# Kernel optimization log

Measured on AMD Instinct MI355X. Metric: run time of the kernel, lower is better.

The kernel has to match this reference:

```python
import jax, jax.numpy as jnp
import numpy as np

N_HEADS, N_KV, HEAD_DIM, D_MODEL, T_MAX = 16, 4, 64, 1024, 2048
GROUPS = N_HEADS // N_KV
EPS = 1e-6


def _rms_norm(x, w):
    # RMSNorm over last dim (head_dim), computed in fp32 like the torch module
    xf = x.astype(jnp.float32)
    r = jax.lax.rsqrt(jnp.mean(xf * xf, axis=-1, keepdims=True) + EPS)
    return (xf * r).astype(x.dtype) * w


def _apply_rope(x, cos, sin):
    # x: (B, H, T, D); cos/sin: (T_max, D/2)
    T = x.shape[2]
    c = cos[:T][None, None]  # (1,1,T,D/2)
    s = sin[:T][None, None]
    x1, x2 = jnp.split(x, 2, axis=-1)
    return jnp.concatenate([x1 * c - x2 * s, x2 * c + x1 * s], axis=-1)


def setup_inputs() -> dict:
    key = jax.random.key(0)
    ks = jax.random.split(key, 8)
    B, T = 2, 2048
    x = jax.random.normal(ks[0], (B, T, D_MODEL), dtype=jnp.float32)
    # realistic RoPE tables
    theta = 10000.0
    inv_freq = 1.0 / (theta ** (np.arange(0, HEAD_DIM, 2, dtype=np.float32) / HEAD_DIM))
    t = np.arange(T_MAX, dtype=np.float32)
    freqs = np.outer(t, inv_freq)  # (T_max, D/2)
    cos = jnp.asarray(np.cos(freqs))
    sin = jnp.asarray(np.sin(freqs))
    sd = 0.02
    wq = jax.random.normal(ks[1], (N_HEADS * HEAD_DIM, D_MODEL), dtype=jnp.float32) * sd
    wk = jax.random.normal(ks[2], (N_KV * HEAD_DIM, D_MODEL), dtype=jnp.float32) * sd
    wv = jax.random.normal(ks[3], (N_KV * HEAD_DIM, D_MODEL), dtype=jnp.float32) * sd
    wo = jax.random.normal(ks[4], (D_MODEL, N_HEADS * HEAD_DIM), dtype=jnp.float32) * sd
    qn_w = jnp.ones((HEAD_DIM,), dtype=jnp.float32)
    kn_w = jnp.ones((HEAD_DIM,), dtype=jnp.float32)
    return {"x": x, "cos": cos, "sin": sin, "wq": wq, "wk": wk, "wv": wv,
            "wo": wo, "qn_w": qn_w, "kn_w": kn_w}


def reference(x, cos, sin, wq, wk, wv, wo, qn_w, kn_w):
    B, T, _ = x.shape
    scale = HEAD_DIM ** -0.5
    # projections (torch Linear: y = x @ W.T)
    q = (x @ wq.T).reshape(B, T, N_HEADS, HEAD_DIM).transpose(0, 2, 1, 3)
    k = (x @ wk.T).reshape(B, T, N_KV, HEAD_DIM).transpose(0, 2, 1, 3)
    v = (x @ wv.T).reshape(B, T, N_KV, HEAD_DIM).transpose(0, 2, 1, 3)
    # qk RMSNorm
    q = _rms_norm(q, qn_w)
    k = _rms_norm(k, kn_w)
    # RoPE
    q = _apply_rope(q, cos, sin)
    k = _apply_rope(k, cos, sin)
    # GQA expansion: query head h uses kv head h // GROUPS
    k = jnp.repeat(k, GROUPS, axis=1)  # (B, H, T, D)
    v = jnp.repeat(v, GROUPS, axis=1)
    # causal SDPA
    scores = jnp.einsum('bhqd,bhkd->bhqk', q, k) * scale
    causal = jnp.tril(jnp.ones((T, T), dtype=bool))
    scores = jnp.where(causal, scores, jnp.finfo(scores.dtype).min)
    p = jax.nn.softmax(scores, axis=-1)
    out = jnp.einsum('bhqk,bhkd->bhqd', p, v)
    out = out.transpose(0, 2, 1, 3).reshape(B, T, N_HEADS * HEAD_DIM)
    return out @ wo.T
```

## Files before the change

kernel.cpp:

```cpp
#include <hip/hip_runtime.h>


typedef __bf16 bf16;
typedef __attribute__((ext_vector_type(8))) __bf16 bf16x8;
typedef __attribute__((ext_vector_type(4))) float f32x4;

#define MFMA(a, b, c) __builtin_amdgcn_mfma_f32_16x16x32_bf16((a), (b), (c), 0, 0, 0)
#define GLOAD_LDS16(g, l)                                        \
  __builtin_amdgcn_global_load_lds(                              \
      (const __attribute__((address_space(1))) void*)(g),        \
      (__attribute__((address_space(3))) void*)(l), 16, 0, 0)

__device__ __forceinline__ bool is_bf16_input(const void* cosRaw) {
  return ((const unsigned short*)cosRaw)[0] == 0x3F80;
}
__device__ __forceinline__ float rdval(const void* p, int idx, bool isbf) {
  return isbf ? (float)((const bf16*)p)[idx] : ((const float*)p)[idx];
}

__device__ __forceinline__ void stage_rows(const void* src, size_t rowbase,
                                           int ko, int srow, int csrc,
                                           int lane, bf16* ls, bool isbf) {
  if (isbf) {
    GLOAD_LDS16(&((const bf16*)src)[(rowbase + srow) * 1024 + ko + csrc * 8], ls);
  } else {
    const float* fp = &((const float*)src)[(rowbase + srow) * 1024 + ko + csrc * 8];
    float4 f0 = *(const float4*)fp;
    float4 f1 = *(const float4*)(fp + 4);
    bf16x8 o;
    o[0] = (bf16)f0.x; o[1] = (bf16)f0.y; o[2] = (bf16)f0.z; o[3] = (bf16)f0.w;
    o[4] = (bf16)f1.x; o[5] = (bf16)f1.y; o[6] = (bf16)f1.z; o[7] = (bf16)f1.w;
    *(bf16x8*)&ls[lane * 8] = o;
  }
}

__global__ __launch_bounds__(256, 6) void proj_kernel(
    const void* __restrict__ xraw, const void* __restrict__ wqraw,
    const void* __restrict__ wkraw, const void* __restrict__ wvraw,
    bf16* __restrict__ qp, bf16* __restrict__ kp, bf16* __restrict__ vt,
    const void* __restrict__ cosraw, const void* __restrict__ sinraw,
    const void* __restrict__ qnraw, const void* __restrict__ knraw) {
  __shared__ bf16 As[64 * 64];
  __shared__ bf16 Bs[64 * 64];

  const int idx = (int)blockIdx.x;
  const int xcd = idx & 7;
  const int jj = idx >> 3;
  const int mb = (jj & 7) * 8 + xcd;
  const int nb = jj >> 3;
  const int n0 = nb * 64;
  const int m0 = mb * 64;

  const int tid = threadIdx.x;
  const int wave = tid >> 6;
  const int lane = tid & 63;
  const int q16 = lane & 15;
  const int quad = lane >> 4;
  const int srow = lane >> 3;
  const int csrc = (lane & 7) ^ srow;
  const int wm = wave * 16;
  const int x7 = q16 & 7;
  const bool isbf = is_bf16_input(cosraw);

  const void* wsrc;
  int nr0;
  if (nb < 16)      { wsrc = wqraw; nr0 = n0; }
  else if (nb < 20) { wsrc = wkraw; nr0 = n0 - 1024; }
  else              { wsrc = wvraw; nr0 = n0 - 1280; }

  f32x4 acc[4];
#pragma unroll
  for (int nt = 0; nt < 4; ++nt) acc[nt] = (f32x4){0.f, 0.f, 0.f, 0.f};

  for (int kt = 0; kt < 16; ++kt) {
    const int ko = kt * 64;
#pragma unroll
    for (int i = 0; i < 2; ++i) {
      int rb = wave * 16 + i * 8;
      stage_rows(xraw, (size_t)(m0 + rb), ko, srow, csrc, lane, &As[rb * 64], isbf);
      stage_rows(wsrc, (size_t)(nr0 + rb), ko, srow, csrc, lane, &Bs[rb * 64], isbf);
    }
    __syncthreads();

    bf16x8 a0, a1, bfr[4][2];
    {
      const bf16* rp = &As[(wm + q16) * 64];
      a0 = *(const bf16x8*)&rp[(quad ^ x7) * 8];
      a1 = *(const bf16x8*)&rp[((quad + 4) ^ x7) * 8];
    }
#pragma unroll
    for (int nt = 0; nt < 4; ++nt) {
      const bf16* rp = &Bs[(nt * 16 + q16) * 64];
      bfr[nt][0] = *(const bf16x8*)&rp[(quad ^ x7) * 8];
      bfr[nt][1] = *(const bf16x8*)&rp[((quad + 4) ^ x7) * 8];
    }
#pragma unroll
    for (int nt = 0; nt < 4; ++nt) {
      acc[nt] = MFMA(a0, bfr[nt][0], acc[nt]);
      acc[nt] = MFMA(a1, bfr[nt][1], acc[nt]);
    }
    __syncthreads();
  }

  if (nb < 20) {
    const void* nwp = (nb < 16) ? qnraw : knraw;
    const float osc = (nb < 16) ? 0.125f : 1.0f;
    float wd[4];
#pragma unroll
    for (int nt = 0; nt < 4; ++nt) wd[nt] = rdval(nwp, nt * 16 + q16, isbf);

#pragma unroll
    for (int r = 0; r < 4; ++r) {
      float p = acc[0][r] * acc[0][r] + acc[1][r] * acc[1][r] +
                acc[2][r] * acc[2][r] + acc[3][r] * acc[3][r];
#pragma unroll
      for (int off = 8; off >= 1; off >>= 1) p += __shfl_xor(p, off);
      float rms = rsqrtf(p * (1.0f / 64.0f) + 1e-6f);

      int row = m0 + wm + quad * 4 + r;
      int t = row & 2047;
      float c0 = rdval(cosraw, t * 32 + q16, isbf);
      float c1 = rdval(cosraw, t * 32 + 16 + q16, isbf);
      float s0 = rdval(sinraw, t * 32 + q16, isbf);
      float s1 = rdval(sinraw, t * 32 + 16 + q16, isbf);

      float v0 = acc[0][r] * rms * wd[0];
      float v1 = acc[1][r] * rms * wd[1];
      float v2 = acc[2][r] * rms * wd[2];
      float v3 = acc[3][r] * rms * wd[3];

      bf16* op = (nb < 16) ? &qp[(size_t)row * 1024 + nb * 64]
                           : &kp[(size_t)row * 256 + (nb - 16) * 64];
      op[0 * 16 + q16] = (bf16)((v0 * c0 - v2 * s0) * osc);
      op[1 * 16 + q16] = (bf16)((v1 * c1 - v3 * s1) * osc);
      op[2 * 16 + q16] = (bf16)((v2 * c0 + v0 * s0) * osc);
      op[3 * 16 + q16] = (bf16)((v3 * c1 + v1 * s1) * osc);
    }
  } else {
    const int vh = nb - 20;
    const int b = m0 >> 11;
    const int tbase = m0 & 2047;
#pragma unroll
    for (int nt = 0; nt < 4; ++nt)
#pragma unroll
      for (int r = 0; r < 4; ++r)
        As[(wm + quad * 4 + r) * 64 + nt * 16 + q16] = (bf16)acc[nt][r];
    __syncthreads();
#pragma unroll
    for (int rep = 0; rep < 2; ++rep) {
      int c = tid + 256 * rep;
      int d = c >> 3;
      int t8 = (c & 7) * 8;
      bf16x8 pk;
#pragma unroll
      for (int j = 0; j < 8; ++j) pk[j] = As[(t8 + j) * 64 + d];
      *(bf16x8*)&vt[(((size_t)(b * 4 + vh)) * 64 + d) * 2048 + tbase + t8] = pk;
    }
  }
}

__global__ __launch_bounds__(256, 2) void flash_kernel(
    const bf16* __restrict__ qp, const bf16* __restrict__ kp,
    const bf16* __restrict__ vt, bf16* __restrict__ attn) {
  const int qblk = blockIdx.z ? 31 - (int)blockIdx.x : (int)blockIdx.x;
  const int hp = blockIdx.y;
  const int b = blockIdx.z;
  const int h0 = hp * 2;
  const int kvh = hp >> 1;
  const int tid = threadIdx.x;
  const int wave = tid >> 6;
  const int lane = tid & 63;
  const int q16 = lane & 15;
  const int quad = lane >> 4;
  const int r7 = q16 & 7;
  const int t0 = qblk * 64 + wave * 16;

  __shared__ bf16 Ks[2][64 * 64];
  __shared__ bf16 Vs[2][64 * 64];
  __shared__ bf16 Pl[4][2][16 * 64];

  bf16x8 qa[2][2];
#pragma unroll
  for (int hd = 0; hd < 2; ++hd) {
    const bf16* qrow =
        qp + (((size_t)(b * 2048 + t0 + q16)) * 16 + h0 + hd) * 64;
    qa[hd][0] = *(const bf16x8*)(qrow + quad * 8);
    qa[hd][1] = *(const bf16x8*)(qrow + 32 + quad * 8);
  }

  bf16x8 ones;
#pragma unroll
  for (int j = 0; j < 8; ++j) ones[j] = (bf16)1.0f;

  f32x4 O[2][4], l4[2];
#pragma unroll
  for (int hd = 0; hd < 2; ++hd) {
#pragma unroll
    for (int nt = 0; nt < 4; ++nt) O[hd][nt] = (f32x4){0.f, 0.f, 0.f, 0.f};
    l4[hd] = (f32x4){0.f, 0.f, 0.f, 0.f};
  }

  const int ntile = qblk + 1;

  bf16x8 kr[2], vr[2];
  const int cr = tid * 2;
  const int krow = cr >> 3;
  const size_t kgbase = (((size_t)(b * 2048) + krow) * 4 + kvh) * 64;
  const size_t vgbase = ((size_t)(b * 4 + kvh) * 64 + krow) * 2048;

  auto gload = [&](int tk) {
#pragma unroll
    for (int rep = 0; rep < 2; ++rep) {
      int ch = (cr + rep) & 7;
      kr[rep] = *(const bf16x8*)&kp[kgbase + (size_t)(tk * 64) * 256 + ch * 8];
      vr[rep] = *(const bf16x8*)&vt[vgbase + tk * 64 + ch * 8];
    }
  };
  auto swrite = [&](int bb) {
#pragma unroll
    for (int rep = 0; rep < 2; ++rep) {
      int ch = (cr + rep) & 7;
      int pos = (ch ^ (krow & 7)) * 8;
      *(bf16x8*)&Ks[bb][krow * 64 + pos] = kr[rep];
      *(bf16x8*)&Vs[bb][krow * 64 + pos] = vr[rep];
    }
  };

  gload(0);

  for (int t = 0; t < ntile; ++t) {
    const int bb = t & 1;
    const int kbase = t * 64;
    swrite(bb);
    __syncthreads();
    if (t + 1 < ntile) gload(t + 1);

    bf16x8 vbr[2][4];
#pragma unroll
    for (int kh = 0; kh < 2; ++kh)
#pragma unroll
      for (int nt = 0; nt < 4; ++nt) {
        const bf16* vr0 = &Vs[bb][(nt * 16 + q16) * 64];
        vbr[kh][nt] = *(const bf16x8*)&vr0[((kh * 4 + quad) ^ r7) * 8];
      }

    bf16x8 kb[4][2];
#pragma unroll
    for (int kt = 0; kt < 4; ++kt) {
      const bf16* kr0 = &Ks[bb][(kt * 16 + q16) * 64];
      kb[kt][0] = *(const bf16x8*)&kr0[(quad ^ r7) * 8];
      kb[kt][1] = *(const bf16x8*)&kr0[((quad + 4) ^ r7) * 8];
    }

    const bool edge = (kbase + 63 > t0);
#pragma unroll
    for (int hd = 0; hd < 2; ++hd) {
      f32x4 s[4];
#pragma unroll
      for (int kt = 0; kt < 4; ++kt) {
        f32x4 z = (f32x4){0.f, 0.f, 0.f, 0.f};
        z = MFMA(qa[hd][0], kb[kt][0], z);
        z = MFMA(qa[hd][1], kb[kt][1], z);
        s[kt] = z;
      }
      if (edge) {
#pragma unroll
        for (int kt = 0; kt < 4; ++kt) {
          int jt = kbase + kt * 16 + q16;
#pragma unroll
          for (int r = 0; r < 4; ++r)
            if (jt > t0 + quad * 4 + r) s[kt][r] = -1e30f;
        }
      }
#pragma unroll
      for (int kt = 0; kt < 4; ++kt)
#pragma unroll
        for (int r = 0; r < 4; ++r) s[kt][r] = __expf(s[kt][r] - 9.0f);

#pragma unroll
      for (int kt = 0; kt < 4; ++kt)
#pragma unroll
        for (int r = 0; r < 4; ++r) {
          int row = quad * 4 + r;
          int col = kt * 16 + q16;
          Pl[wave][hd][row * 64 + ((col >> 3) ^ (row & 7)) * 8 + (col & 7)] =
              (bf16)s[kt][r];
        }
    }

#pragma unroll
    for (int hd = 0; hd < 2; ++hd)
#pragma unroll
      for (int kh = 0; kh < 2; ++kh) {
        bf16x8 pa = *(const bf16x8*)&Pl[wave][hd][q16 * 64 +
                                                  (((kh * 4 + quad) ^ r7) * 8)];
#pragma unroll
        for (int nt = 0; nt < 4; ++nt)
          O[hd][nt] = MFMA(pa, vbr[kh][nt], O[hd][nt]);
        l4[hd] = MFMA(pa, ones, l4[hd]);
      }
  }

#pragma unroll
  for (int hd = 0; hd < 2; ++hd) {
    float inv[4];
#pragma unroll
    for (int r = 0; r < 4; ++r) inv[r] = 1.0f / l4[hd][r];
#pragma unroll
    for (int nt = 0; nt < 4; ++nt)
#pragma unroll
      for (int r = 0; r < 4; ++r) {
        size_t o = (((size_t)(b * 2048 + t0 + quad * 4 + r)) * 16 + h0 + hd) * 64 +
                   nt * 16 + q16;
        attn[o] = (bf16)(O[hd][nt][r] * inv[r]);
      }
  }
}

__global__ __launch_bounds__(256, 6) void gemm_o_kernel(
    const bf16* __restrict__ A, const void* __restrict__ Wraw,
    void* __restrict__ C, const void* __restrict__ cosraw) {
  __shared__ bf16 As[64 * 64];
  __shared__ bf16 Bs[64 * 64];

  const int idx = (int)blockIdx.x;
  const int xcd = idx & 7;
  const int jj = idx >> 3;
  const int mb = (jj & 7) * 8 + xcd;
  const int nb = jj >> 3;
  const int n0 = nb * 64;
  const int m0 = mb * 64;

  const int tid = threadIdx.x;
  const int wave = tid >> 6;
  const int lane = tid & 63;
  const int q16 = lane & 15;
  const int quad = lane >> 4;
  const int srow = lane >> 3;
  const int csrc = (lane & 7) ^ srow;
  const int wm = wave * 16;
  const int x7 = q16 & 7;
  const bool isbf = is_bf16_input(cosraw);

  f32x4 acc[4];
#pragma unroll
  for (int nt = 0; nt < 4; ++nt) acc[nt] = (f32x4){0.f, 0.f, 0.f, 0.f};

  for (int kt = 0; kt < 16; ++kt) {
    const int ko = kt * 64;
#pragma unroll
    for (int i = 0; i < 2; ++i) {
      int rb = wave * 16 + i * 8;
      GLOAD_LDS16(&A[(size_t)(m0 + rb + srow) * 1024 + ko + csrc * 8],
                  &As[rb * 64]);
      stage_rows(Wraw, (size_t)(n0 + rb), ko, srow, csrc, lane, &Bs[rb * 64], isbf);
    }
    __syncthreads();

    bf16x8 a0, a1, bfr[4][2];
    {
      const bf16* rp = &As[(wm + q16) * 64];
      a0 = *(const bf16x8*)&rp[(quad ^ x7) * 8];
      a1 = *(const bf16x8*)&rp[((quad + 4) ^ x7) * 8];
    }
#pragma unroll
    for (int nt = 0; nt < 4; ++nt) {
      const bf16* rp = &Bs[(nt * 16 + q16) * 64];
      bfr[nt][0] = *(const bf16x8*)&rp[(quad ^ x7) * 8];
      bfr[nt][1] = *(const bf16x8*)&rp[((quad + 4) ^ x7) * 8];
    }
#pragma unroll
    for (int nt = 0; nt < 4; ++nt) {
      acc[nt] = MFMA(a0, bfr[nt][0], acc[nt]);
      acc[nt] = MFMA(a1, bfr[nt][1], acc[nt]);
    }
    __syncthreads();
  }

#pragma unroll
  for (int nt = 0; nt < 4; ++nt)
#pragma unroll
    for (int r = 0; r < 4; ++r) {
      size_t idx2 = (size_t)(m0 + wm + quad * 4 + r) * 1024 + n0 + nt * 16 + q16;
      if (isbf) ((bf16*)C)[idx2] = (bf16)acc[nt][r];
      else      ((float*)C)[idx2] = acc[nt][r];
    }
}

extern "C" void kernel_launch(void* const* d_in, const int* in_sizes, int n_in,
                              void* d_out, int out_size, void* d_ws, size_t ws_size,
                              hipStream_t stream) {
  bf16* qp = (bf16*)d_ws;
  bf16* kp = qp + (size_t)4096 * 1024;
  bf16* vt = kp + (size_t)4096 * 256;
  bf16* at = vt + (size_t)4096 * 256;

  proj_kernel<<<1536, 256, 0, stream>>>(
      d_in[0], d_in[3], d_in[4], d_in[5], qp, kp, vt,
      d_in[1], d_in[2], d_in[7], d_in[8]);

  flash_kernel<<<dim3(32, 8, 2), 256, 0, stream>>>(qp, kp, vt, at);

  gemm_o_kernel<<<1024, 256, 0, stream>>>(at, d_in[6], d_out, d_in[1]);
}
```

Before: 176.8 us.

## Process one head per flash block to double grid and occupancy

The flash attention kernel now handles a single query head per block instead of two heads sharing a KV tile. The grid doubles along the head dimension and launch bounds rise to 4 blocks per CU. The P tile is written and consumed in 32-column halves interleaved with the PV MFMAs, which shrinks the LDS and register footprint. The trade-off is that each K/V tile is loaded from global memory twice as often, since two heads no longer share one staged tile.

```diff
diff --git a/kernel.cpp b/kernel.cpp
--- a/kernel.cpp
+++ b/kernel.cpp
@@ -159,14 +159,13 @@
   }
 }
 
-__global__ __launch_bounds__(256, 2) void flash_kernel(
+__global__ __launch_bounds__(256, 4) void flash_kernel(
     const bf16* __restrict__ qp, const bf16* __restrict__ kp,
     const bf16* __restrict__ vt, bf16* __restrict__ attn) {
   const int qblk = blockIdx.z ? 31 - (int)blockIdx.x : (int)blockIdx.x;
-  const int hp = blockIdx.y;
+  const int h = blockIdx.y;
   const int b = blockIdx.z;
-  const int h0 = hp * 2;
-  const int kvh = hp >> 1;
+  const int kvh = h >> 2;
   const int tid = threadIdx.x;
   const int wave = tid >> 6;
   const int lane = tid & 63;
@@ -177,28 +176,20 @@
 
   __shared__ bf16 Ks[2][64 * 64];
   __shared__ bf16 Vs[2][64 * 64];
-  __shared__ bf16 Pl[4][2][16 * 64];
-
-  bf16x8 qa[2][2];
-#pragma unroll
-  for (int hd = 0; hd < 2; ++hd) {
-    const bf16* qrow =
-        qp + (((size_t)(b * 2048 + t0 + q16)) * 16 + h0 + hd) * 64;
-    qa[hd][0] = *(const bf16x8*)(qrow + quad * 8);
-    qa[hd][1] = *(const bf16x8*)(qrow + 32 + quad * 8);
-  }
+  __shared__ bf16 Pl[4][16 * 32];
+
+  const bf16* qrow = qp + (((size_t)(b * 2048 + t0 + q16)) * 16 + h) * 64;
+  bf16x8 qa0 = *(const bf16x8*)(qrow + quad * 8);
+  bf16x8 qa1 = *(const bf16x8*)(qrow + 32 + quad * 8);
 
   bf16x8 ones;
 #pragma unroll
   for (int j = 0; j < 8; ++j) ones[j] = (bf16)1.0f;
 
-  f32x4 O[2][4], l4[2];
-#pragma unroll
-  for (int hd = 0; hd < 2; ++hd) {
-#pragma unroll
-    for (int nt = 0; nt < 4; ++nt) O[hd][nt] = (f32x4){0.f, 0.f, 0.f, 0.f};
-    l4[hd] = (f32x4){0.f, 0.f, 0.f, 0.f};
-  }
+  f32x4 O[4], l4;
+#pragma unroll
+  for (int nt = 0; nt < 4; ++nt) O[nt] = (f32x4){0.f, 0.f, 0.f, 0.f};
+  l4 = (f32x4){0.f, 0.f, 0.f, 0.f};
 
   const int ntile = qblk + 1;
 
@@ -235,86 +226,68 @@
     __syncthreads();
     if (t + 1 < ntile) gload(t + 1);
 
-    bf16x8 vbr[2][4];
-#pragma unroll
-    for (int kh = 0; kh < 2; ++kh)
+    f32x4 s[4];
+#pragma unroll
+    for (int kt = 0; kt < 4; ++kt) {
+      const bf16* kr0 = &Ks[bb][(kt * 16 + q16) * 64];
+      bf16x8 kb0 = *(const bf16x8*)&kr0[(quad ^ r7) * 8];
+      bf16x8 kb1 = *(const bf16x8*)&kr0[((quad + 4) ^ r7) * 8];
+      f32x4 z = (f32x4){0.f, 0.f, 0.f, 0.f};
+      z = MFMA(qa0, kb0, z);
+      z = MFMA(qa1, kb1, z);
+      s[kt] = z;
+    }
+
+    if (kbase + 63 > t0) {
+#pragma unroll
+      for (int kt = 0; kt < 4; ++kt) {
+        int jt = kbase + kt * 16 + q16;
+#pragma unroll
+        for (int r = 0; r < 4; ++r)
+          if (jt > t0 + quad * 4 + r) s[kt][r] = -1e30f;
+      }
+    }
+
+#pragma unroll
+    for (int kt = 0; kt < 4; ++kt)
+#pragma unroll
+      for (int r = 0; r < 4; ++r) s[kt][r] = __expf(s[kt][r] - 9.0f);
+
+#pragma unroll
+    for (int kh = 0; kh < 2; ++kh) {
+#pragma unroll
+      for (int ct = 0; ct < 2; ++ct) {
+        const int kt = kh * 2 + ct;
+#pragma unroll
+        for (int r = 0; r < 4; ++r) {
+          int row = quad * 4 + r;
+          int col = ct * 16 + q16;
+          Pl[wave][row * 32 + (((col >> 3) ^ (row & 3)) * 8) + (col & 7)] =
+              (bf16)s[kt][r];
+        }
+      }
+      bf16x8 pa = *(const bf16x8*)&Pl[wave][q16 * 32 + ((quad ^ (q16 & 3)) * 8)];
 #pragma unroll
       for (int nt = 0; nt < 4; ++nt) {
         const bf16* vr0 = &Vs[bb][(nt * 16 + q16) * 64];
-        vbr[kh][nt] = *(const bf16x8*)&vr0[((kh * 4 + quad) ^ r7) * 8];
+        bf16x8 vb = *(const bf16x8*)&vr0[((kh * 4 + quad) ^ r7) * 8];
+        O[nt] = MFMA(pa, vb, O[nt]);
       }
-
-    bf16x8 kb[4][2];
-#pragma unroll
-    for (int kt = 0; kt < 4; ++kt) {
-      const bf16* kr0 = &Ks[bb][(kt * 16 + q16) * 64];
-      kb[kt][0] = *(const bf16x8*)&kr0[(quad ^ r7) * 8];
-      kb[kt][1] = *(const bf16x8*)&kr0[((quad + 4) ^ r7) * 8];
-    }
-
-    const bool edge = (kbase + 63 > t0);
-#pragma unroll
-    for (int hd = 0; hd < 2; ++hd) {
-      f32x4 s[4];
-#pragma unroll
-      for (int kt = 0; kt < 4; ++kt) {
-        f32x4 z = (f32x4){0.f, 0.f, 0.f, 0.f};
-        z = MFMA(qa[hd][0], kb[kt][0], z);
-        z = MFMA(qa[hd][1], kb[kt][1], z);
-        s[kt] = z;
-      }
-      if (edge) {
-#pragma unroll
-        for (int kt = 0; kt < 4; ++kt) {
-          int jt = kbase + kt * 16 + q16;
-#pragma unroll
-          for (int r = 0; r < 4; ++r)
-            if (jt > t0 + quad * 4 + r) s[kt][r] = -1e30f;
-        }
-      }
-#pragma unroll
-      for (int kt = 0; kt < 4; ++kt)
-#pragma unroll
-        for (int r = 0; r < 4; ++r) s[kt][r] = __expf(s[kt][r] - 9.0f);
-
-#pragma unroll
-      for (int kt = 0; kt < 4; ++kt)
-#pragma unroll
-        for (int r = 0; r < 4; ++r) {
-          int row = quad * 4 + r;
-          int col = kt * 16 + q16;
-          Pl[wave][hd][row * 64 + ((col >> 3) ^ (row & 7)) * 8 + (col & 7)] =
-              (bf16)s[kt][r];
-        }
-    }
-
-#pragma unroll
-    for (int hd = 0; hd < 2; ++hd)
-#pragma unroll
-      for (int kh = 0; kh < 2; ++kh) {
-        bf16x8 pa = *(const bf16x8*)&Pl[wave][hd][q16 * 64 +
-                                                  (((kh * 4 + quad) ^ r7) * 8)];
-#pragma unroll
-        for (int nt = 0; nt < 4; ++nt)
-          O[hd][nt] = MFMA(pa, vbr[kh][nt], O[hd][nt]);
-        l4[hd] = MFMA(pa, ones, l4[hd]);
-      }
-  }
-
-#pragma unroll
-  for (int hd = 0; hd < 2; ++hd) {
-    float inv[4];
-#pragma unroll
-    for (int r = 0; r < 4; ++r) inv[r] = 1.0f / l4[hd][r];
-#pragma unroll
-    for (int nt = 0; nt < 4; ++nt)
-#pragma unroll
-      for (int r = 0; r < 4; ++r) {
-        size_t o = (((size_t)(b * 2048 + t0 + quad * 4 + r)) * 16 + h0 + hd) * 64 +
-                   nt * 16 + q16;
-        attn[o] = (bf16)(O[hd][nt][r] * inv[r]);
-      }
-  }
+      l4 = MFMA(pa, ones, l4);
+    }
+  }
+
+  float inv[4];
+#pragma unroll
+  for (int r = 0; r < 4; ++r) inv[r] = 1.0f / l4[r];
+#pragma unroll
+  for (int nt = 0; nt < 4; ++nt)
+#pragma unroll
+    for (int r = 0; r < 4; ++r) {
+      size_t o = (((size_t)(b * 2048 + t0 + quad * 4 + r)) * 16 + h) * 64 +
+                 nt * 16 + q16;
+      attn[o] = (bf16)(O[nt][r] * inv[r]);
+    }
 }
 
 __global__ __launch_bounds__(256, 6) void gemm_o_kernel(
@@ -399,7 +372,7 @@
       d_in[0], d_in[3], d_in[4], d_in[5], qp, kp, vt,
       d_in[1], d_in[2], d_in[7], d_in[8]);
 
-  flash_kernel<<<dim3(32, 8, 2), 256, 0, stream>>>(qp, kp, vt, at);
+  flash_kernel<<<dim3(32, 16, 2), 256, 0, stream>>>(qp, kp, vt, at);
 
   gemm_o_kernel<<<1024, 256, 0, stream>>>(at, d_in[6], d_out, d_in[1]);
 }
```

Measured after the change: 172.8 us. 1.02x faster.
